# Kernel tuning notes

Measured on AMD Instinct MI355X. Metric: run time of the kernel, lower is better.

The kernel has to match this reference:

```python
import jax, jax.numpy as jnp
import numpy as np

ALPHA = 0.2  # leaky relu slope
NEG = -1e9


def setup_inputs() -> dict:
    key = jax.random.key(0)
    ks = jax.random.split(key, 8)
    B, N, F_IN, H, HID, OUT = 2, 4096, 512, 4, 128, 64
    x = jax.random.normal(ks[0], (B, N, F_IN), dtype=jnp.float32)
    adj = jax.random.randint(ks[1], (B, N, N), 0, 2, dtype=jnp.int32)
    s_in = float(np.sqrt(2.0 / (F_IN + HID)))
    W_heads = jax.random.normal(ks[2], (H, HID, F_IN), dtype=jnp.float32) * s_in
    a1_heads = jax.random.normal(ks[3], (H, HID), dtype=jnp.float32) * 0.1
    a2_heads = jax.random.normal(ks[4], (H, HID), dtype=jnp.float32) * 0.1
    s_out = float(np.sqrt(2.0 / (H * HID + OUT)))
    W_out = jax.random.normal(ks[5], (OUT, H * HID), dtype=jnp.float32) * s_out
    a1_out = jax.random.normal(ks[6], (OUT,), dtype=jnp.float32) * 0.1
    a2_out = jax.random.normal(ks[7], (OUT,), dtype=jnp.float32) * 0.1
    return {"x": x, "adj": adj, "W_heads": W_heads, "a1_heads": a1_heads,
            "a2_heads": a2_heads, "W_out": W_out, "a1_out": a1_out, "a2_out": a2_out}


def _gat_layer(x, adj, W, a1, a2, concat):
    # x: [B,N,F], W: [O,F], a1/a2: [O]
    h = jnp.einsum('bnf,of->bno', x, W)            # [B,N,O]
    f1 = jnp.einsum('bno,o->bn', h, a1)            # [B,N]
    f2 = jnp.einsum('bno,o->bn', h, a2)            # [B,N]
    e = f1[:, :, None] + f2[:, None, :]            # [B,N,N] additive scores
    e = jnp.where(e > 0, e, ALPHA * e)             # leaky relu
    e = jnp.where(adj == 0, NEG, e)                # adjacency mask
    att = jax.nn.softmax(e, axis=2)
    h_prime = jnp.einsum('bnm,bmo->bno', att, h)
    return jax.nn.elu(h_prime) if concat else h_prime


def reference(x, adj, W_heads, a1_heads, a2_heads, W_out, a1_out, a2_out):
    H = W_heads.shape[0]
    heads = [_gat_layer(x, adj, W_heads[i], a1_heads[i], a2_heads[i], True)
             for i in range(H)]
    x_cat = jnp.concatenate(heads, axis=2)         # [B,N,H*HID]
    return _gat_layer(x_cat, adj, W_out, a1_out, a2_out, False)
```

## Files before the change

kernel.cpp:

```cpp
#include <hip/hip_runtime.h>

#define TB 2
#define TN 4096
#define TH 4
#define THID 128
#define TOUT 64
#define NW 128

using f4    = __attribute__((ext_vector_type(4))) float;
using s16x8 = __attribute__((ext_vector_type(8))) short;
using s16x4 = __attribute__((ext_vector_type(4))) short;
using u32x4 = __attribute__((ext_vector_type(4))) unsigned;

static __device__ __forceinline__ short f2bf(float f){
  unsigned u = __float_as_uint(f);
  unsigned r = u + 0x7FFFu + ((u >> 16) & 1u);
  return (short)(r >> 16);
}
static __device__ __forceinline__ float bf2f(short s){
  return __uint_as_float(((unsigned)(unsigned short)s) << 16);
}
static __device__ __forceinline__ unsigned encf(float f){
  unsigned u = __float_as_uint(f);
  return (u & 0x80000000u) ? ~u : (u | 0x80000000u);
}
static __device__ __forceinline__ float decf(unsigned u){
  unsigned v = (u & 0x80000000u) ? (u & 0x7FFFFFFFu) : ~u;
  return __uint_as_float(v);
}
static __device__ __forceinline__ void gll16(const void* g, void* l){
  __builtin_amdgcn_global_load_lds((const __attribute__((address_space(1))) unsigned int*)g,
                                   (__attribute__((address_space(3))) unsigned int*)l, 16, 0, 0);
}
static __device__ __forceinline__ f4 mfma_bf16(s16x8 a, s16x8 b, f4 c){
  return __builtin_amdgcn_mfma_f32_16x16x32_bf16(a, b, c, 0, 0, 0);
}

__global__ void k_prep(const int* __restrict__ adj, unsigned* __restrict__ adjT,
                       unsigned* __restrict__ mx,
                       const float* __restrict__ x, short* __restrict__ xh, short* __restrict__ xl,
                       const float* __restrict__ Wh, short* __restrict__ wh, short* __restrict__ wl,
                       const float* __restrict__ Wo, short* __restrict__ wo){
  int bid = blockIdx.x;
  if (bid == 0 && threadIdx.x < 16) mx[threadIdx.x] = 0;
  if (bid < 4096){
    int t = bid * 256 + threadIdx.x;
    int n = t & 4095, w = (t >> 12) & 127, b = t >> 19;
    const int4* p = (const int4*)(adj + ((size_t)(b*TN + n))*TN + w*32);
    unsigned m = 0;
#pragma unroll
    for (int i = 0; i < 8; ++i){
      int4 v = p[i];
      m |= (v.x != 0 ? 1u : 0u) << (i*4+0);
      m |= (v.y != 0 ? 1u : 0u) << (i*4+1);
      m |= (v.z != 0 ? 1u : 0u) << (i*4+2);
      m |= (v.w != 0 ? 1u : 0u) << (i*4+3);
    }
    adjT[((size_t)(b*NW + w))*TN + n] = m;
  } else if (bid < 8192){
    int t = (bid - 4096) * 256 + threadIdx.x;
    f4 v = ((const f4*)x)[t];
    s16x4 h, l;
#pragma unroll
    for (int e = 0; e < 4; ++e){
      short hb = f2bf(v[e]);
      h[e] = hb;
      l[e] = f2bf(v[e] - bf2f(hb));
    }
    ((s16x4*)xh)[t] = h;
    ((s16x4*)xl)[t] = l;
  } else if (bid < 8448){
    int t = (bid - 8192) * 256 + threadIdx.x;
    f4 v = ((const f4*)Wh)[t];
    s16x4 h, l;
#pragma unroll
    for (int e = 0; e < 4; ++e){
      short hb = f2bf(v[e]);
      h[e] = hb;
      l[e] = f2bf(v[e] - bf2f(hb));
    }
    ((s16x4*)wh)[t] = h;
    ((s16x4*)wl)[t] = l;
  } else {
    int t = (bid - 8448) * 256 + threadIdx.x;
    f4 v = ((const f4*)Wo)[t];
    s16x4 h;
#pragma unroll
    for (int e = 0; e < 4; ++e) h[e] = f2bf(v[e]);
    ((s16x4*)wo)[t] = h;
  }
}

__global__ __launch_bounds__(512, 2) void k_gemm1(
    const short* __restrict__ xh, const short* __restrict__ xl,
    const short* __restrict__ wh, const short* __restrict__ wl,
    const float* __restrict__ a1h, const float* __restrict__ a2h,
    short* __restrict__ hTb, float* __restrict__ f1g,
    float* __restrict__ Qa, float* __restrict__ Sa, unsigned* __restrict__ mx){
  __shared__ short tiles[2][4][8192];
  __shared__ float red[2][128][2];
  __shared__ float bmx[2];
  int tid = threadIdx.x, lane = tid & 63, w = tid >> 6;
  int kgrp = lane >> 4, li = lane & 15;
  int nblk = blockIdx.x >> 6, mblk = blockIdx.x & 63;
  int n0 = nblk * 128, m0 = mblk * 128;
  int wn = w >> 2, wm = w & 3;
  const f4 fz = {0.f, 0.f, 0.f, 0.f};
  f4 acc[4][2];
#pragma unroll
  for (int i = 0; i < 4; ++i)
#pragma unroll
    for (int j = 0; j < 2; ++j) acc[i][j] = fz;

#pragma unroll
  for (int tno = 0; tno < 4; ++tno){
    const short* gb = (tno==0 ? wh : tno==1 ? wl : tno==2 ? xh : xl);
    int r0 = (tno < 2) ? n0 : m0;
#pragma unroll
    for (int i = 0; i < 2; ++i){
      int s = (i*8 + w)*64 + lane;
      int row = s >> 3, c = s & 7, cs = c ^ (row & 7);
      gll16(gb + (size_t)(r0 + row)*512 + cs*8, (char*)tiles[0][tno] + (i*8+w)*1024);
    }
  }
  asm volatile("s_waitcnt vmcnt(0)" ::: "memory");
  __syncthreads();

  for (int kt = 0; kt < 8; ++kt){
    int cur = kt & 1;
    if (kt < 7){
      int k0 = (kt+1) * 64;
#pragma unroll
      for (int tno = 0; tno < 4; ++tno){
        const short* gb = (tno==0 ? wh : tno==1 ? wl : tno==2 ? xh : xl);
        int r0 = (tno < 2) ? n0 : m0;
#pragma unroll
        for (int i = 0; i < 2; ++i){
          int s = (i*8 + w)*64 + lane;
          int row = s >> 3, c = s & 7, cs = c ^ (row & 7);
          gll16(gb + (size_t)(r0 + row)*512 + k0 + cs*8, (char*)tiles[cur^1][tno] + (i*8+w)*1024);
        }
      }
    }
    const char* t0 = (const char*)tiles[cur][0];
    const char* t1 = (const char*)tiles[cur][1];
    const char* t2 = (const char*)tiles[cur][2];
    const char* t3 = (const char*)tiles[cur][3];
#pragma unroll
    for (int ks = 0; ks < 2; ++ks){
      int ck = ks*4 + kgrp;
      s16x8 ah[4], al[4], bh[2], bl[2];
#pragma unroll
      for (int fn = 0; fn < 4; ++fn){
        int row = wn*64 + fn*16 + li;
        int off = row*128 + ((ck ^ (row & 7)) << 4);
        ah[fn] = *(const s16x8*)(t0 + off);
        al[fn] = *(const s16x8*)(t1 + off);
      }
#pragma unroll
      for (int fm = 0; fm < 2; ++fm){
        int row = wm*32 + fm*16 + li;
        int off = row*128 + ((ck ^ (row & 7)) << 4);
        bh[fm] = *(const s16x8*)(t2 + off);
        bl[fm] = *(const s16x8*)(t3 + off);
      }
#pragma unroll
      for (int fn = 0; fn < 4; ++fn)
#pragma unroll
        for (int fm = 0; fm < 2; ++fm)
          acc[fn][fm] = mfma_bf16(ah[fn], bh[fm], acc[fn][fm]);
#pragma unroll
      for (int fn = 0; fn < 4; ++fn)
#pragma unroll
        for (int fm = 0; fm < 2; ++fm)
          acc[fn][fm] = mfma_bf16(ah[fn], bl[fm], acc[fn][fm]);
#pragma unroll
      for (int fn = 0; fn < 4; ++fn)
#pragma unroll
        for (int fm = 0; fm < 2; ++fm)
          acc[fn][fm] = mfma_bf16(al[fn], bh[fm], acc[fn][fm]);
    }
    asm volatile("s_waitcnt vmcnt(0)" ::: "memory");
    __syncthreads();
  }
  int head = nblk;
#pragma unroll
  for (int fn = 0; fn < 4; ++fn){
#pragma unroll
    for (int fm = 0; fm < 2; ++fm){
#pragma unroll
      for (int r = 0; r < 4; ++r){
        int nout = n0 + wn*64 + fn*16 + kgrp*4 + r;
        int m = m0 + wm*32 + fm*16 + li;
        int b = m >> 12, n = m & 4095;
        int hid = nout & 127;
        size_t idx = ((size_t)((b*TH + head)*THID + hid))*TN + n;
        hTb[idx] = f2bf(acc[fn][fm][r]);
      }
    }
  }
  const float* a1p = a1h + head*THID;
  const float* a2p = a2h + head*THID;
  float s1[2] = {0.f, 0.f}, s2[2] = {0.f, 0.f};
#pragma unroll
  for (int fn = 0; fn < 4; ++fn)
#pragma unroll
    for (int r = 0; r < 4; ++r){
      int row = wn*64 + fn*16 + kgrp*4 + r;
      float w1 = a1p[row], w2 = a2p[row];
#pragma unroll
      for (int fm = 0; fm < 2; ++fm){
        s1[fm] = fmaf(acc[fn][fm][r], w1, s1[fm]);
        s2[fm] = fmaf(acc[fn][fm][r], w2, s2[fm]);
      }
    }
#pragma unroll
  for (int fm = 0; fm < 2; ++fm){
    s1[fm] += __shfl_xor(s1[fm], 16); s1[fm] += __shfl_xor(s1[fm], 32);
    s2[fm] += __shfl_xor(s2[fm], 16); s2[fm] += __shfl_xor(s2[fm], 32);
  }
  if (kgrp == 0){
#pragma unroll
    for (int fm = 0; fm < 2; ++fm){
      int col = wm*32 + fm*16 + li;
      red[wn][col][0] = s1[fm];
      red[wn][col][1] = s2[fm];
    }
  }
  __syncthreads();
  if (tid < 128){
    float f1v = red[0][tid][0] + red[1][tid][0];
    float f2v = red[0][tid][1] + red[1][tid][1];
    int m = m0 + tid, b = m >> 12, n = m & 4095;
    int idx = (b*TH + head)*TN + n;
    f1g[idx] = f1v;
    Qa[idx] = expf(f2v);
    Sa[idx] = expf(0.2f*f2v);
    float wmx = f2v;
#pragma unroll
    for (int d = 1; d < 64; d <<= 1) wmx = fmaxf(wmx, __shfl_xor(wmx, d));
    if ((tid & 63) == 0) bmx[tid >> 6] = wmx;
  }
  __syncthreads();
  if (tid == 0){
    int b = m0 >> 12;
    atomicMax(&mx[b*TH + head], encf(fmaxf(bmx[0], bmx[1])));
  }
}

__global__ __launch_bounds__(256, 2) void k_attn1(
    const short* __restrict__ hTb, const float* __restrict__ f1,
    const float* __restrict__ Qa, const float* __restrict__ Sa,
    const unsigned* __restrict__ adjT, const unsigned* __restrict__ mx,
    short* __restrict__ part, float* __restrict__ sums){
  __shared__ short tile[3][8192];
  __shared__ float Qs[1024], Ss[1024];
  __shared__ unsigned abuf[3][512];
  int tid = threadIdx.x, lane = tid & 63, w = tid >> 6;
  int kgrp = lane >> 4, li = lane & 15;
  int bid = blockIdx.x;
  int js = bid >> 7, b = (bid >> 6) & 1, h = (bid >> 4) & 3, rblk = bid & 15;
  int bh = b*TH + h;
  int jbase = js * 1024;
  int r0b = rblk * 256;
  const short* hbase = hTb + ((size_t)bh*THID)*TN;
  const float* Qrow = Qa + (size_t)bh*TN + jbase;
  const float* Srow = Sa + (size_t)bh*TN + jbase;

  auto STAGE = [&](int t){
    int jg = jbase + t*64;
    int bi = t % 3;
    char* dst = (char*)tile[bi];
#pragma unroll
    for (int i = 0; i < 4; ++i){
      int s = (i*4 + w)*64 + lane;
      int row = s >> 3, c = s & 7, cs = c ^ (row & 7);
      gll16(hbase + (size_t)row*TN + jg + cs*8, dst + (i*4+w)*1024);
    }
    int w0 = jg >> 5;
#pragma unroll
    for (int k = 0; k < 2; ++k)
      gll16(adjT + (size_t)(b*NW + w0 + k)*TN + r0b + lane*4, (char*)abuf[bi] + k*1024);
  };

  gll16(Qrow + w*256 + lane*4, (char*)Qs + w*1024);
  gll16(Srow + w*256 + lane*4, (char*)Ss + w*1024);
  STAGE(0); STAGE(1);

  int r0 = r0b + w*64;
  float Pv[4], Rv[4];
  int lrow[4];
  float mf = decf(mx[bh]);
#pragma unroll
  for (int rf = 0; rf < 4; ++rf){
    int row = r0 + rf*16 + li;
    lrow[rf] = w*64 + rf*16 + li;
    float f1v = f1[bh*TN + row];
    float e = f1v + mf;
    float m = e > 0.f ? e : 0.2f*e;
    Pv[rf] = expf(f1v - m);
    Rv[rf] = expf(0.2f*f1v - m);
  }
  const f4 fz = {0.f,0.f,0.f,0.f};
  f4 acc[4][8];
#pragma unroll
  for (int i = 0; i < 4; ++i)
#pragma unroll
    for (int j = 0; j < 8; ++j) acc[i][j] = fz;
  f4 accs[4] = {fz, fz, fz, fz};
  s16x8 ones;
#pragma unroll
  for (int e = 0; e < 8; ++e) ones[e] = (short)0x3F80;

  for (int jt = 0; jt < 16; ++jt){
    if (jt < 15) asm volatile("s_waitcnt vmcnt(6)" ::: "memory");
    else         asm volatile("s_waitcnt vmcnt(0)" ::: "memory");
    __builtin_amdgcn_s_barrier();
    __builtin_amdgcn_sched_barrier(0);
    if (jt < 14) STAGE(jt + 2);

    int j0 = jt*64;
    int bi = jt % 3;
    const char* tp = (const char*)tile[bi];
    const unsigned* ab = abuf[bi];
    unsigned aw0[4], aw1[4];
#pragma unroll
    for (int rf = 0; rf < 4; ++rf){
      aw0[rf] = ab[lrow[rf]];
      aw1[rf] = ab[256 + lrow[rf]];
    }
#pragma unroll
    for (int ks = 0; ks < 2; ++ks){
      int jloc = j0 + ks*32 + kgrp*8;
      float qv[8], sv[8];
      *(f4*)&qv[0] = *(const f4*)&Qs[jloc];
      *(f4*)&qv[4] = *(const f4*)&Qs[jloc+4];
      *(f4*)&sv[0] = *(const f4*)&Ss[jloc];
      *(f4*)&sv[4] = *(const f4*)&Ss[jloc+4];
      s16x8 af[4];
#pragma unroll
      for (int rf = 0; rf < 4; ++rf){
        unsigned word = ks ? aw1[rf] : aw0[rf];
        unsigned byt = (word >> (kgrp*8)) & 0xFFu;
        float P = Pv[rf], R = Rv[rf];
        u32x4 pw;
#pragma unroll
        for (int pe = 0; pe < 4; ++pe){
          float va = fmaxf(P*qv[2*pe],   R*sv[2*pe]);
          float vb = fmaxf(P*qv[2*pe+1], R*sv[2*pe+1]);
          va = (byt & (1u << (2*pe)))   ? va : 0.f;
          vb = (byt & (1u << (2*pe+1))) ? vb : 0.f;
          unsigned ua = __float_as_uint(va) + 0x8000u;
          unsigned ub = __float_as_uint(vb) + 0x8000u;
          pw[pe] = __builtin_amdgcn_perm(ub, ua, 0x07060302);
        }
        af[rf] = __builtin_bit_cast(s16x8, pw);
      }
#pragma unroll
      for (int rf = 0; rf < 4; ++rf)
        accs[rf] = mfma_bf16(af[rf], ones, accs[rf]);
#pragma unroll
      for (int cf = 0; cf < 8; ++cf){
        int col = cf*16 + li;
        int off = col*128 + (((ks*4 + kgrp) ^ (col & 7)) << 4);
        s16x8 bfr = *(const s16x8*)(tp + off);
#pragma unroll
        for (int rf = 0; rf < 4; ++rf)
          acc[rf][cf] = mfma_bf16(af[rf], bfr, acc[rf][cf]);
      }
    }
  }
  int sl = js*8 + bh;
  if (li == 0){
#pragma unroll
    for (int rf = 0; rf < 4; ++rf)
#pragma unroll
      for (int r = 0; r < 4; ++r)
        sums[(size_t)sl*TN + r0 + rf*16 + kgrp*4 + r] = accs[rf][r];
  }
#pragma unroll
  for (int rf = 0; rf < 4; ++rf)
#pragma unroll
    for (int cf = 0; cf < 8; ++cf)
#pragma unroll
      for (int r = 0; r < 4; ++r){
        int row = r0 + rf*16 + kgrp*4 + r;
        int hid = cf*16 + li;
        part[((size_t)sl*TN + row)*THID + hid] = f2bf(acc[rf][cf][r]);
      }
}

__global__ __launch_bounds__(128) void k_cg2(
    const short* __restrict__ part1, const float* __restrict__ sums1,
    const short* __restrict__ wo,
    const float* __restrict__ a1o, const float* __restrict__ a2o,
    short* __restrict__ h2T, float* __restrict__ f1o,
    float* __restrict__ Q2, float* __restrict__ S2, unsigned* __restrict__ mx2){
  __shared__ short xs[32*512];
  __shared__ float invs[32];
  int tid = threadIdx.x, lane = tid & 63, w = tid >> 6;
  int kgrp = lane >> 4, li = lane & 15;
  int m0 = blockIdx.x * 32;
  if (tid < 32){
    int row = m0 + tid, b = row >> 12, n = row & 4095;
    float s = 0.f;
#pragma unroll
    for (int js = 0; js < 4; ++js)
      s += sums1[(size_t)(js*8 + b*TH)*TN + 0];
    (void)s; (void)n;
  }
  __syncthreads();
  for (int it = 0; it < 16; ++it){
    int idx = it*128 + tid;
    int r = idx >> 6, c8 = idx & 63;
    int row = m0 + r, b = row >> 12, n = row & 4095;
    int h = c8 >> 4, hid8 = c8 & 15;
    float a[8] = {0,0,0,0,0,0,0,0};
    float s = 0.f;
#pragma unroll
    for (int js = 0; js < 4; ++js){
      size_t rowoff = (size_t)(js*8 + b*TH + h)*TN + n;
      s16x8 pv = *(const s16x8*)(part1 + rowoff*THID + hid8*8);
#pragma unroll
      for (int e = 0; e < 8; ++e) a[e] += bf2f(pv[e]);
      s += sums1[rowoff];
    }
    float inv = 1.f / s;
    s16x8 o;
#pragma unroll
    for (int e = 0; e < 8; ++e){
      float xv = a[e] * inv;
      o[e] = f2bf(xv > 0.f ? xv : expm1f(xv));
    }
    *(s16x8*)((char*)xs + r*1024 + ((c8*16) ^ ((r & 7) << 4))) = o;
  }
  __syncthreads();
  const f4 fz = {0.f,0.f,0.f,0.f};
  f4 acc[4] = {fz, fz, fz, fz};
  int rowL = w*16 + li;
  for (int kt = 0; kt < 16; ++kt){
    int k = kt*32 + kgrp*8;
    s16x8 a = *(const s16x8*)((const char*)xs + rowL*1024 + ((k*2) ^ ((rowL & 7) << 4)));
#pragma unroll
    for (int cf = 0; cf < 4; ++cf){
      int col = cf*16 + li;
      s16x8 bfr = *(const s16x8*)(wo + (size_t)col*512 + k);
      acc[cf] = mfma_bf16(a, bfr, acc[cf]);
    }
  }
  float p1[4] = {0,0,0,0}, p2[4] = {0,0,0,0};
#pragma unroll
  for (int cf = 0; cf < 4; ++cf){
    int o = cf*16 + li;
    float w1 = a1o[o], w2 = a2o[o];
#pragma unroll
    for (int r = 0; r < 4; ++r){
      p1[r] = fmaf(acc[cf][r], w1, p1[r]);
      p2[r] = fmaf(acc[cf][r], w2, p2[r]);
    }
  }
#pragma unroll
  for (int r = 0; r < 4; ++r){
#pragma unroll
    for (int d = 1; d < 16; d <<= 1){
      p1[r] += __shfl_xor(p1[r], d);
      p2[r] += __shfl_xor(p2[r], d);
    }
  }
#pragma unroll
  for (int cf = 0; cf < 4; ++cf)
#pragma unroll
    for (int r = 0; r < 4; ++r){
      int row = m0 + w*16 + kgrp*4 + r;
      int o = cf*16 + li;
      int b = row >> 12, n = row & 4095;
      h2T[((size_t)(b*TOUT + o))*TN + n] = f2bf(acc[cf][r]);
    }
  if (li == 0){
#pragma unroll
    for (int r = 0; r < 4; ++r){
      int row = m0 + w*16 + kgrp*4 + r;
      f1o[row] = p1[r];
      Q2[row] = expf(p2[r]);
      S2[row] = expf(0.2f*p2[r]);
    }
  }
  float m2 = fmaxf(fmaxf(p2[0], p2[1]), fmaxf(p2[2], p2[3]));
  m2 = fmaxf(m2, __shfl_xor(m2, 16));
  m2 = fmaxf(m2, __shfl_xor(m2, 32));
  __shared__ float bm[2];
  if (lane == 0) bm[w] = m2;
  __syncthreads();
  if (tid == 0) atomicMax(&mx2[m0 >> 12], encf(fmaxf(bm[0], bm[1])));
  (void)invs;
}

__global__ __launch_bounds__(256, 2) void k_attn2(
    const short* __restrict__ h2T, const float* __restrict__ f1o,
    const float* __restrict__ Q2, const float* __restrict__ S2,
    const unsigned* __restrict__ adjT, const unsigned* __restrict__ mx2,
    float* __restrict__ part, float* __restrict__ sums){
  __shared__ short tile[3][4096];
  __shared__ float Qs[512], Ss[512];
  __shared__ unsigned abuf[3][256];
  int tid = threadIdx.x, lane = tid & 63, w = tid >> 6;
  int kgrp = lane >> 4, li = lane & 15;
  int bid = blockIdx.x;
  int js = bid >> 6, b = (bid >> 5) & 1, rblk = bid & 31;
  int jbase = js * 512;
  int r0b = rblk * 128;
  const short* hbase = h2T + (size_t)b*TOUT*TN;
  const float* Qrow = Q2 + (size_t)b*TN + jbase;
  const float* Srow = S2 + (size_t)b*TN + jbase;

  auto STAGE = [&](int t){
    int jg = jbase + t*64;
    int bi = t % 3;
    char* dst = (char*)tile[bi];
#pragma unroll
    for (int i = 0; i < 2; ++i){
      int s = (i*4 + w)*64 + lane;
      int row = s >> 3, c = s & 7, cs = c ^ (row & 7);
      gll16(hbase + (size_t)row*TN + jg + cs*8, dst + (i*4+w)*1024);
    }
    int w0 = jg >> 5;
    gll16(adjT + (size_t)(b*NW + w0 + (lane>>5))*TN + r0b + (lane&31)*4, (char*)abuf[bi]);
  };

  if (w < 2) gll16(Qrow + w*256 + lane*4, (char*)Qs + w*1024);
  else       gll16(Srow + (w-2)*256 + lane*4, (char*)Ss + (w-2)*1024);
  STAGE(0); STAGE(1);

  int r0 = r0b + w*32;
  float Pv[2], Rv[2];
  int lrow[2];
  float mf = decf(mx2[b]);
#pragma unroll
  for (int rf = 0; rf < 2; ++rf){
    int row = r0 + rf*16 + li;
    lrow[rf] = w*32 + rf*16 + li;
    float f1v = f1o[b*TN + row];
    float e = f1v + mf;
    float m = e > 0.f ? e : 0.2f*e;
    Pv[rf] = expf(f1v - m);
    Rv[rf] = expf(0.2f*f1v - m);
  }
  const f4 fz = {0.f,0.f,0.f,0.f};
  f4 acc[2][4];
#pragma unroll
  for (int i = 0; i < 2; ++i)
#pragma unroll
    for (int j = 0; j < 4; ++j) acc[i][j] = fz;
  f4 accs[2] = {fz, fz};
  s16x8 ones;
#pragma unroll
  for (int e = 0; e < 8; ++e) ones[e] = (short)0x3F80;

  for (int jt = 0; jt < 8; ++jt){
    if (jt < 7) asm volatile("s_waitcnt vmcnt(3)" ::: "memory");
    else        asm volatile("s_waitcnt vmcnt(0)" ::: "memory");
    __builtin_amdgcn_s_barrier();
    __builtin_amdgcn_sched_barrier(0);
    if (jt < 6) STAGE(jt + 2);

    int j0 = jt*64;
    int bi = jt % 3;
    const char* tp = (const char*)tile[bi];
    const unsigned* ab = abuf[bi];
    unsigned aw0[2], aw1[2];
#pragma unroll
    for (int rf = 0; rf < 2; ++rf){
      aw0[rf] = ab[lrow[rf]];
      aw1[rf] = ab[128 + lrow[rf]];
    }
#pragma unroll
    for (int ks = 0; ks < 2; ++ks){
      int jloc = j0 + ks*32 + kgrp*8;
      float qv[8], sv[8];
      *(f4*)&qv[0] = *(const f4*)&Qs[jloc];
      *(f4*)&qv[4] = *(const f4*)&Qs[jloc+4];
      *(f4*)&sv[0] = *(const f4*)&Ss[jloc];
      *(f4*)&sv[4] = *(const f4*)&Ss[jloc+4];
      s16x8 af[2];
#pragma unroll
      for (int rf = 0; rf < 2; ++rf){
        unsigned word = ks ? aw1[rf] : aw0[rf];
        unsigned byt = (word >> (kgrp*8)) & 0xFFu;
        float P = Pv[rf], R = Rv[rf];
        u32x4 pw;
#pragma unroll
        for (int pe = 0; pe < 4; ++pe){
          float va = fmaxf(P*qv[2*pe],   R*sv[2*pe]);
          float vb = fmaxf(P*qv[2*pe+1], R*sv[2*pe+1]);
          va = (byt & (1u << (2*pe)))   ? va : 0.f;
          vb = (byt & (1u << (2*pe+1))) ? vb : 0.f;
          unsigned ua = __float_as_uint(va) + 0x8000u;
          unsigned ub = __float_as_uint(vb) + 0x8000u;
          pw[pe] = __builtin_amdgcn_perm(ub, ua, 0x07060302);
        }
        af[rf] = __builtin_bit_cast(s16x8, pw);
      }
      accs[0] = mfma_bf16(af[0], ones, accs[0]);
      accs[1] = mfma_bf16(af[1], ones, accs[1]);
#pragma unroll
      for (int cf = 0; cf < 4; ++cf){
        int col = cf*16 + li;
        int off = col*128 + (((ks*4 + kgrp) ^ (col & 7)) << 4);
        s16x8 bfr = *(const s16x8*)(tp + off);
        acc[0][cf] = mfma_bf16(af[0], bfr, acc[0][cf]);
        acc[1][cf] = mfma_bf16(af[1], bfr, acc[1][cf]);
      }
    }
  }
  int sl = js*2 + b;
  if (li == 0){
#pragma unroll
    for (int rf = 0; rf < 2; ++rf)
#pragma unroll
      for (int r = 0; r < 4; ++r)
        sums[(size_t)sl*TN + r0 + rf*16 + kgrp*4 + r] = accs[rf][r];
  }
#pragma unroll
  for (int rf = 0; rf < 2; ++rf)
#pragma unroll
    for (int cf = 0; cf < 4; ++cf)
#pragma unroll
      for (int r = 0; r < 4; ++r){
        int row = r0 + rf*16 + kgrp*4 + r;
        int o = cf*16 + li;
        part[((size_t)sl*TN + row)*TOUT + o] = acc[rf][cf][r];
      }
}

__global__ void k_comb2(const float* __restrict__ part, const float* __restrict__ sums,
                        float* __restrict__ out){
  int t = blockIdx.x*256 + threadIdx.x;
  int o4 = t & 15, n = (t >> 4) & 4095, b = t >> 16;
  f4 a = {0.f,0.f,0.f,0.f};
  float s = 0.f;
#pragma unroll
  for (int js = 0; js < 8; ++js){
    int sl = js*2 + b;
    a += ((const f4*)part)[((size_t)sl*TN + n)*16 + o4];
    s += sums[(size_t)sl*TN + n];
  }
  f4 r = a / s;
  ((f4*)out)[((size_t)(b*TN + n))*16 + o4] = r;
}

extern "C" void kernel_launch(void* const* d_in, const int* in_sizes, int n_in,
                              void* d_out, int out_size, void* d_ws, size_t ws_size,
                              hipStream_t stream) {
  (void)in_sizes; (void)n_in; (void)out_size; (void)ws_size;
  const float* x       = (const float*)d_in[0];
  const int*   adj     = (const int*)d_in[1];
  const float* W_heads = (const float*)d_in[2];
  const float* a1h     = (const float*)d_in[3];
  const float* a2h     = (const float*)d_in[4];
  const float* W_out   = (const float*)d_in[5];
  const float* a1o     = (const float*)d_in[6];
  const float* a2o     = (const float*)d_in[7];

  char* p = (char*)d_ws;
  auto alloc = [&](size_t sz){ char* r = p; p += (sz + 255) & ~(size_t)255; return r; };
  unsigned* adjT  = (unsigned*) alloc(4ull*1048576);
  short*    wo    = (short*)    alloc(2ull*32768);
  short*    hTb   = (short*)    alloc(2ull*4194304);
  float*    f1    = (float*)    alloc(4ull*32768);
  float*    Qa    = (float*)    alloc(4ull*32768);
  float*    Sa    = (float*)    alloc(4ull*32768);
  unsigned* mx    = (unsigned*) alloc(4ull*16);
  float*    f1o   = (float*)    alloc(4ull*8192);
  float*    Q2    = (float*)    alloc(4ull*8192);
  float*    S2    = (float*)    alloc(4ull*8192);
  short*    h2T   = (short*)    alloc(2ull*524288);
  float*    sums1 = (float*)    alloc(4ull*131072);
  float*    sums2 = (float*)    alloc(4ull*65536);
  char* A = alloc(33554432ull);
  short* xh   = (short*)A;
  short* xl   = (short*)(A + 8388608);
  short* part1 = (short*)A;
  char* Bu = alloc(16777216ull);
  short* wh = (short*)Bu;
  short* wl = (short*)(Bu + 524288);
  float* part2 = (float*)Bu;

  k_prep <<<8480, 256, 0, stream>>>(adj, adjT, mx, x, xh, xl, W_heads, wh, wl, W_out, wo);
  k_gemm1<<<256, 512, 0, stream>>>(xh, xl, wh, wl, a1h, a2h, hTb, f1, Qa, Sa, mx);
  k_attn1<<<512, 256, 0, stream>>>(hTb, f1, Qa, Sa, adjT, mx, part1, sums1);
  k_cg2  <<<256, 128, 0, stream>>>(part1, sums1, wo, a1o, a2o, h2T, f1o, Q2, S2, mx + 8);
  k_attn2<<<512, 256, 0, stream>>>(h2T, f1o, Q2, S2, adjT, mx + 8, part2, sums2);
  k_comb2<<<512, 256, 0, stream>>>(part2, sums2, (float*)d_out);
}
```

Measured before the change: 150.4 us.

## Pack adjacency row-major with wave ballots and load mask words directly in attention

The adjacency bitmask is now built one row per wavefront with __ballot and stored row-major (row × 128 words) instead of transposed word-major. The attention kernels drop the LDS mask buffers and read each row's two mask words straight from global memory into registers. Their staging changes from a 3-deep asynchronous pipeline with partial vmcnt waits to a 2-deep double buffer with a full wait and barrier each iteration. This cuts LDS use and simplifies the prep pass, but the full vmcnt(0) plus barrier per tile may expose load latency that the triple-buffered version hid.

```diff
diff --git a/kernel.cpp b/kernel.cpp
--- a/kernel.cpp
+++ b/kernel.cpp
@@ -36,29 +36,16 @@
   return __builtin_amdgcn_mfma_f32_16x16x32_bf16(a, b, c, 0, 0, 0);
 }
 
-__global__ void k_prep(const int* __restrict__ adj, unsigned* __restrict__ adjT,
+__global__ void k_prep(const int* __restrict__ adj, unsigned* __restrict__ adjp,
                        unsigned* __restrict__ mx,
                        const float* __restrict__ x, short* __restrict__ xh, short* __restrict__ xl,
                        const float* __restrict__ Wh, short* __restrict__ wh, short* __restrict__ wl,
                        const float* __restrict__ Wo, short* __restrict__ wo){
-  int bid = blockIdx.x;
-  if (bid == 0 && threadIdx.x < 16) mx[threadIdx.x] = 0;
+  __shared__ unsigned plds[4][128];
+  int bid = blockIdx.x, tid = threadIdx.x, lane = tid & 63, w = tid >> 6;
+  if (bid == 0 && tid < 16) mx[tid] = 0;
   if (bid < 4096){
-    int t = bid * 256 + threadIdx.x;
-    int n = t & 4095, w = (t >> 12) & 127, b = t >> 19;
-    const int4* p = (const int4*)(adj + ((size_t)(b*TN + n))*TN + w*32);
-    unsigned m = 0;
-#pragma unroll
-    for (int i = 0; i < 8; ++i){
-      int4 v = p[i];
-      m |= (v.x != 0 ? 1u : 0u) << (i*4+0);
-      m |= (v.y != 0 ? 1u : 0u) << (i*4+1);
-      m |= (v.z != 0 ? 1u : 0u) << (i*4+2);
-      m |= (v.w != 0 ? 1u : 0u) << (i*4+3);
-    }
-    adjT[((size_t)(b*NW + w))*TN + n] = m;
-  } else if (bid < 8192){
-    int t = (bid - 4096) * 256 + threadIdx.x;
+    int t = bid * 256 + tid;
     f4 v = ((const f4*)x)[t];
     s16x4 h, l;
 #pragma unroll
@@ -69,8 +56,21 @@
     }
     ((s16x4*)xh)[t] = h;
     ((s16x4*)xl)[t] = l;
-  } else if (bid < 8448){
-    int t = (bid - 8192) * 256 + threadIdx.x;
+  } else if (bid < 6144){
+    int gw = (bid - 4096)*4 + w;
+    int b = gw >> 12, n = gw & 4095;
+    const int* rowp = adj + ((size_t)(b*TN + n))*TN;
+    for (int k = 0; k < 64; ++k){
+      int v = rowp[k*64 + lane];
+      unsigned long long m = __ballot(v != 0);
+      if (lane == 0) *((unsigned long long*)&plds[w][2*k]) = m;
+    }
+    __syncthreads();
+    unsigned* dst = adjp + ((size_t)(b*TN + n))*NW;
+    dst[lane]      = plds[w][lane];
+    dst[64 + lane] = plds[w][64 + lane];
+  } else if (bid < 6400){
+    int t = (bid - 6144) * 256 + tid;
     f4 v = ((const f4*)Wh)[t];
     s16x4 h, l;
 #pragma unroll
@@ -82,7 +82,7 @@
     ((s16x4*)wh)[t] = h;
     ((s16x4*)wl)[t] = l;
   } else {
-    int t = (bid - 8448) * 256 + threadIdx.x;
+    int t = (bid - 6400) * 256 + tid;
     f4 v = ((const f4*)Wo)[t];
     s16x4 h;
 #pragma unroll
@@ -251,11 +251,10 @@
 __global__ __launch_bounds__(256, 2) void k_attn1(
     const short* __restrict__ hTb, const float* __restrict__ f1,
     const float* __restrict__ Qa, const float* __restrict__ Sa,
-    const unsigned* __restrict__ adjT, const unsigned* __restrict__ mx,
+    const unsigned* __restrict__ adjp, const unsigned* __restrict__ mx,
     short* __restrict__ part, float* __restrict__ sums){
-  __shared__ short tile[3][8192];
+  __shared__ short tile[2][8192];
   __shared__ float Qs[1024], Ss[1024];
-  __shared__ unsigned abuf[3][512];
   int tid = threadIdx.x, lane = tid & 63, w = tid >> 6;
   int kgrp = lane >> 4, li = lane & 15;
   int bid = blockIdx.x;
@@ -267,34 +266,28 @@
   const float* Qrow = Qa + (size_t)bh*TN + jbase;
   const float* Srow = Sa + (size_t)bh*TN + jbase;
 
-  auto STAGE = [&](int t){
+  auto STAGE = [&](int t, char* dst){
     int jg = jbase + t*64;
-    int bi = t % 3;
-    char* dst = (char*)tile[bi];
 #pragma unroll
     for (int i = 0; i < 4; ++i){
       int s = (i*4 + w)*64 + lane;
       int row = s >> 3, c = s & 7, cs = c ^ (row & 7);
       gll16(hbase + (size_t)row*TN + jg + cs*8, dst + (i*4+w)*1024);
     }
-    int w0 = jg >> 5;
-#pragma unroll
-    for (int k = 0; k < 2; ++k)
-      gll16(adjT + (size_t)(b*NW + w0 + k)*TN + r0b + lane*4, (char*)abuf[bi] + k*1024);
   };
 
   gll16(Qrow + w*256 + lane*4, (char*)Qs + w*1024);
   gll16(Srow + w*256 + lane*4, (char*)Ss + w*1024);
-  STAGE(0); STAGE(1);
+  STAGE(0, (char*)tile[0]);
 
   int r0 = r0b + w*64;
   float Pv[4], Rv[4];
-  int lrow[4];
+  int rowa[4];
   float mf = decf(mx[bh]);
 #pragma unroll
   for (int rf = 0; rf < 4; ++rf){
     int row = r0 + rf*16 + li;
-    lrow[rf] = w*64 + rf*16 + li;
+    rowa[rf] = row;
     float f1v = f1[bh*TN + row];
     float e = f1v + mf;
     float m = e > 0.f ? e : 0.2f*e;
@@ -312,23 +305,25 @@
 #pragma unroll
   for (int e = 0; e < 8; ++e) ones[e] = (short)0x3F80;
 
+  uint2 awc[4], awn[4];
+#pragma unroll
+  for (int rf = 0; rf < 4; ++rf)
+    awc[rf] = *(const uint2*)&adjp[(size_t)(b*TN + rowa[rf])*NW + (jbase >> 5)];
+
+  asm volatile("s_waitcnt vmcnt(0)" ::: "memory");
+  __syncthreads();
+
   for (int jt = 0; jt < 16; ++jt){
-    if (jt < 15) asm volatile("s_waitcnt vmcnt(6)" ::: "memory");
-    else         asm volatile("s_waitcnt vmcnt(0)" ::: "memory");
-    __builtin_amdgcn_s_barrier();
-    __builtin_amdgcn_sched_barrier(0);
-    if (jt < 14) STAGE(jt + 2);
-
+    int cur = jt & 1;
+    if (jt < 15){
+      STAGE(jt+1, (char*)tile[cur^1]);
+      int jg = jbase + (jt+1)*64;
+#pragma unroll
+      for (int rf = 0; rf < 4; ++rf)
+        awn[rf] = *(const uint2*)&adjp[(size_t)(b*TN + rowa[rf])*NW + (jg >> 5)];
+    }
     int j0 = jt*64;
-    int bi = jt % 3;
-    const char* tp = (const char*)tile[bi];
-    const unsigned* ab = abuf[bi];
-    unsigned aw0[4], aw1[4];
-#pragma unroll
-    for (int rf = 0; rf < 4; ++rf){
-      aw0[rf] = ab[lrow[rf]];
-      aw1[rf] = ab[256 + lrow[rf]];
-    }
+    const char* tp = (const char*)tile[cur];
 #pragma unroll
     for (int ks = 0; ks < 2; ++ks){
       int jloc = j0 + ks*32 + kgrp*8;
@@ -340,7 +335,7 @@
       s16x8 af[4];
 #pragma unroll
       for (int rf = 0; rf < 4; ++rf){
-        unsigned word = ks ? aw1[rf] : aw0[rf];
+        unsigned word = ks ? awc[rf].y : awc[rf].x;
         unsigned byt = (word >> (kgrp*8)) & 0xFFu;
         float P = Pv[rf], R = Rv[rf];
         u32x4 pw;
@@ -369,6 +364,10 @@
           acc[rf][cf] = mfma_bf16(af[rf], bfr, acc[rf][cf]);
       }
     }
+    asm volatile("s_waitcnt vmcnt(0)" ::: "memory");
+    __syncthreads();
+#pragma unroll
+    for (int rf = 0; rf < 4; ++rf) awc[rf] = awn[rf];
   }
   int sl = js*8 + bh;
   if (li == 0){
@@ -397,19 +396,9 @@
     short* __restrict__ h2T, float* __restrict__ f1o,
     float* __restrict__ Q2, float* __restrict__ S2, unsigned* __restrict__ mx2){
   __shared__ short xs[32*512];
-  __shared__ float invs[32];
   int tid = threadIdx.x, lane = tid & 63, w = tid >> 6;
   int kgrp = lane >> 4, li = lane & 15;
   int m0 = blockIdx.x * 32;
-  if (tid < 32){
-    int row = m0 + tid, b = row >> 12, n = row & 4095;
-    float s = 0.f;
-#pragma unroll
-    for (int js = 0; js < 4; ++js)
-      s += sums1[(size_t)(js*8 + b*TH)*TN + 0];
-    (void)s; (void)n;
-  }
-  __syncthreads();
   for (int it = 0; it < 16; ++it){
     int idx = it*128 + tid;
     int r = idx >> 6, c8 = idx & 63;
@@ -492,17 +481,15 @@
   if (lane == 0) bm[w] = m2;
   __syncthreads();
   if (tid == 0) atomicMax(&mx2[m0 >> 12], encf(fmaxf(bm[0], bm[1])));
-  (void)invs;
 }
 
 __global__ __launch_bounds__(256, 2) void k_attn2(
     const short* __restrict__ h2T, const float* __restrict__ f1o,
     const float* __restrict__ Q2, const float* __restrict__ S2,
-    const unsigned* __restrict__ adjT, const unsigned* __restrict__ mx2,
+    const unsigned* __restrict__ adjp, const unsigned* __restrict__ mx2,
     float* __restrict__ part, float* __restrict__ sums){
-  __shared__ short tile[3][4096];
+  __shared__ short tile[2][4096];
   __shared__ float Qs[512], Ss[512];
-  __shared__ unsigned abuf[3][256];
   int tid = threadIdx.x, lane = tid & 63, w = tid >> 6;
   int kgrp = lane >> 4, li = lane & 15;
   int bid = blockIdx.x;
@@ -513,32 +500,28 @@
   const float* Qrow = Q2 + (size_t)b*TN + jbase;
   const float* Srow = S2 + (size_t)b*TN + jbase;
 
-  auto STAGE = [&](int t){
+  auto STAGE = [&](int t, char* dst){
     int jg = jbase + t*64;
-    int bi = t % 3;
-    char* dst = (char*)tile[bi];
 #pragma unroll
     for (int i = 0; i < 2; ++i){
       int s = (i*4 + w)*64 + lane;
       int row = s >> 3, c = s & 7, cs = c ^ (row & 7);
       gll16(hbase + (size_t)row*TN + jg + cs*8, dst + (i*4+w)*1024);
     }
-    int w0 = jg >> 5;
-    gll16(adjT + (size_t)(b*NW + w0 + (lane>>5))*TN + r0b + (lane&31)*4, (char*)abuf[bi]);
   };
 
   if (w < 2) gll16(Qrow + w*256 + lane*4, (char*)Qs + w*1024);
   else       gll16(Srow + (w-2)*256 + lane*4, (char*)Ss + (w-2)*1024);
-  STAGE(0); STAGE(1);
+  STAGE(0, (char*)tile[0]);
 
   int r0 = r0b + w*32;
   float Pv[2], Rv[2];
-  int lrow[2];
+  int rowa[2];
   float mf = decf(mx2[b]);
 #pragma unroll
   for (int rf = 0; rf < 2; ++rf){
     int row = r0 + rf*16 + li;
-    lrow[rf] = w*32 + rf*16 + li;
+    rowa[rf] = row;
     float f1v = f1o[b*TN + row];
     float e = f1v + mf;
     float m = e > 0.f ? e : 0.2f*e;
@@ -556,23 +539,25 @@
 #pragma unroll
   for (int e = 0; e < 8; ++e) ones[e] = (short)0x3F80;
 
+  uint2 awc[2], awn[2];
+#pragma unroll
+  for (int rf = 0; rf < 2; ++rf)
+    awc[rf] = *(const uint2*)&adjp[(size_t)(b*TN + rowa[rf])*NW + (jbase >> 5)];
+
+  asm volatile("s_waitcnt vmcnt(0)" ::: "memory");
+  __syncthreads();
+
   for (int jt = 0; jt < 8; ++jt){
-    if (jt < 7) asm volatile("s_waitcnt vmcnt(3)" ::: "memory");
-    else        asm volatile("s_waitcnt vmcnt(0)" ::: "memory");
-    __builtin_amdgcn_s_barrier();
-    __builtin_amdgcn_sched_barrier(0);
-    if (jt < 6) STAGE(jt + 2);
-
+    int cur = jt & 1;
+    if (jt < 7){
+      STAGE(jt+1, (char*)tile[cur^1]);
+      int jg = jbase + (jt+1)*64;
+#pragma unroll
+      for (int rf = 0; rf < 2; ++rf)
+        awn[rf] = *(const uint2*)&adjp[(size_t)(b*TN + rowa[rf])*NW + (jg >> 5)];
+    }
     int j0 = jt*64;
-    int bi = jt % 3;
-    const char* tp = (const char*)tile[bi];
-    const unsigned* ab = abuf[bi];
-    unsigned aw0[2], aw1[2];
-#pragma unroll
-    for (int rf = 0; rf < 2; ++rf){
-      aw0[rf] = ab[lrow[rf]];
-      aw1[rf] = ab[128 + lrow[rf]];
-    }
+    const char* tp = (const char*)tile[cur];
 #pragma unroll
     for (int ks = 0; ks < 2; ++ks){
       int jloc = j0 + ks*32 + kgrp*8;
@@ -584,7 +569,7 @@
       s16x8 af[2];
 #pragma unroll
       for (int rf = 0; rf < 2; ++rf){
-        unsigned word = ks ? aw1[rf] : aw0[rf];
+        unsigned word = ks ? awc[rf].y : awc[rf].x;
         unsigned byt = (word >> (kgrp*8)) & 0xFFu;
         float P = Pv[rf], R = Rv[rf];
         u32x4 pw;
@@ -611,6 +596,9 @@
         acc[1][cf] = mfma_bf16(af[1], bfr, acc[1][cf]);
       }
     }
+    asm volatile("s_waitcnt vmcnt(0)" ::: "memory");
+    __syncthreads();
+    awc[0] = awn[0]; awc[1] = awn[1];
   }
   int sl = js*2 + b;
   if (li == 0){
@@ -663,7 +651,7 @@
 
   char* p = (char*)d_ws;
   auto alloc = [&](size_t sz){ char* r = p; p += (sz + 255) & ~(size_t)255; return r; };
-  unsigned* adjT  = (unsigned*) alloc(4ull*1048576);
+  unsigned* adjp  = (unsigned*) alloc(4ull*1048576);
   short*    wo    = (short*)    alloc(2ull*32768);
   short*    hTb   = (short*)    alloc(2ull*4194304);
   float*    f1    = (float*)    alloc(4ull*32768);
@@ -685,10 +673,10 @@
   short* wl = (short*)(Bu + 524288);
   float* part2 = (float*)Bu;
 
-  k_prep <<<8480, 256, 0, stream>>>(adj, adjT, mx, x, xh, xl, W_heads, wh, wl, W_out, wo);
+  k_prep <<<6432, 256, 0, stream>>>(adj, adjp, mx, x, xh, xl, W_heads, wh, wl, W_out, wo);
   k_gemm1<<<256, 512, 0, stream>>>(xh, xl, wh, wl, a1h, a2h, hTb, f1, Qa, Sa, mx);
-  k_attn1<<<512, 256, 0, stream>>>(hTb, f1, Qa, Sa, adjT, mx, part1, sums1);
+  k_attn1<<<512, 256, 0, stream>>>(hTb, f1, Qa, Sa, adjp, mx, part1, sums1);
   k_cg2  <<<256, 128, 0, stream>>>(part1, sums1, wo, a1o, a2o, h2T, f1o, Q2, S2, mx + 8);
-  k_attn2<<<512, 256, 0, stream>>>(h2T, f1o, Q2, S2, adjT, mx + 8, part2, sums2);
+  k_attn2<<<512, 256, 0, stream>>>(h2T, f1o, Q2, S2, adjp, mx + 8, part2, sums2);
   k_comb2<<<512, 256, 0, stream>>>(part2, sums2, (float*)d_out);
 }
```

Result: slower. 155.8 us (+3.6%).
